# Performance work log

Hardware: AMD Instinct MI355X
Metric: run time of the kernel (lower is better)

## Reference

```python
import jax, jax.numpy as jnp
import numpy as np

B, S, E, H = 2, 2048, 1024, 16
D = E // H          # head_dim = 64
HK = H // 4         # heads per kernel group = 4
MASKED_BIAS = -10000.0


def _dwconv_causal(x, w, b):
    # x: [B, h, S, D], w: [D, k], b: [D]; causal depthwise conv along S
    k = w.shape[1]
    s = x.shape[2]
    xp = jnp.pad(x, ((0, 0), (0, 0), (k - 1, 0), (0, 0)))
    out = b
    for i in range(k):
        out = out + xp[:, :, i:i + s, :] * w[:, i]
    return out


def setup_inputs() -> dict:
    key = jax.random.key(0)
    ks = jax.random.split(key, 32)
    inp = {
        'hidden_states': jax.random.normal(ks[0], (B, S, E), jnp.float32),
        'c_attn_w': jax.random.normal(ks[1], (E, 3 * E), jnp.float32) * 0.02,
        'c_attn_b': jnp.zeros((3 * E,), jnp.float32),
        'c_proj_w': jax.random.normal(ks[2], (E, E), jnp.float32) * 0.02,
        'c_proj_b': jnp.zeros((E,), jnp.float32),
    }
    i = 3
    for pre in ('q', 'k', 'v'):
        for kern in (3, 5, 7):
            inp[f'{pre}w{kern}'] = jax.random.normal(ks[i], (D, kern), jnp.float32) * (1.0 / kern)
            inp[f'{pre}b{kern}'] = jnp.zeros((D,), jnp.float32)
            i += 1
    return inp


def _forward(hidden_states, c_attn_w, c_attn_b, c_proj_w, c_proj_b,
             qw3, qb3, qw5, qb5, qw7, qb7,
             kw3, kb3, kw5, kb5, kw7, kb7,
             vw3, vb3, vw5, vb5, vw7, vb7):
    qkv = hidden_states @ c_attn_w + c_attn_b            # [B,S,3E]
    q, k, v = jnp.split(qkv, 3, axis=-1)

    def split_heads(t):
        return t.reshape(B, S, H, D).transpose(0, 2, 1, 3)  # [B,H,S,D]

    q, k, v = split_heads(q), split_heads(k), split_heads(v)

    def tranception_mix(t, ws_bs):
        parts = [t[:, :HK]]
        for g, (w, b) in enumerate(ws_bs):
            parts.append(_dwconv_causal(t[:, (g + 1) * HK:(g + 2) * HK], w, b))
        return jnp.concatenate(parts, axis=1)

    q = tranception_mix(q, [(qw3, qb3), (qw5, qb5), (qw7, qb7)])
    k = tranception_mix(k, [(kw3, kb3), (kw5, kb5), (kw7, kb7)])
    v = tranception_mix(v, [(vw3, vb3), (vw5, vb5), (vw7, vb7)])

    scores = jnp.einsum('bhqd,bhkd->bhqk', q, k) / jnp.sqrt(jnp.float32(D))
    causal = jnp.tril(jnp.ones((S, S), bool))
    scores = jnp.where(causal, scores, jnp.float32(MASKED_BIAS))
    attn = jax.nn.softmax(scores, axis=-1)
    out = jnp.einsum('bhqk,bhkd->bhqd', attn, v)
    out = out.transpose(0, 2, 1, 3).reshape(B, S, E)
    return out @ c_proj_w + c_proj_b


def reference(hidden_states, c_attn_w, c_attn_b, c_proj_w, c_proj_b,
              qw3, qb3, qw5, qb5, qw7, qb7,
              kw3, kb3, kw5, kb5, kw7, kb7,
              vw3, vb3, vw5, vb5, vw7, vb7):
    return _forward(hidden_states, c_attn_w, c_attn_b, c_proj_w, c_proj_b,
                    qw3, qb3, qw5, qb5, qw7, qb7,
                    kw3, kb3, kw5, kb5, kw7, kb7,
                    vw3, vb3, vw5, vb5, vw7, vb7)
```

## Files before the change

### kernel.cpp

```cpp
#include <hip/hip_runtime.h>
#include <stdint.h>
#include <math.h>

typedef unsigned short u16;
typedef __attribute__((ext_vector_type(8))) short short8;
typedef __attribute__((ext_vector_type(4))) float floatx4;

#define DEV static __device__ __forceinline__

struct alignas(8) us4 { u16 x, y, z, w; };
struct alignas(16) us8 { u16 v[8]; };
struct alignas(16) f4 { float x, y, z, w; };
struct alignas(8) f2 { float x, y; };
struct alignas(8) u32x2 { uint32_t x, y; };

DEV u16 f2bf(float f) {
  uint32_t u = __float_as_uint(f);
  u += 0x7fffu + ((u >> 16) & 1u);
  return (u16)(u >> 16);
}
DEV float bf2f(u16 h) { return __uint_as_float(((uint32_t)h) << 16); }

DEV uint32_t pkbf(float a, float b) {
#if __has_builtin(__builtin_amdgcn_cvt_pk_bf16_f32)
  typedef __attribute__((ext_vector_type(2))) __bf16 bf2_t;
  bf2_t v = __builtin_amdgcn_cvt_pk_bf16_f32(a, b);
  uint32_t r; __builtin_memcpy(&r, &v, 4); return r;
#else
  return (uint32_t)f2bf(a) | ((uint32_t)f2bf(b) << 16);
#endif
}

DEV float fexp2(float x) {
#if __has_builtin(__builtin_amdgcn_exp2f)
  return __builtin_amdgcn_exp2f(x);
#else
  return exp2f(x);
#endif
}

DEV void load_lds16(const void* g, void* l) {
  __builtin_amdgcn_global_load_lds((const __attribute__((address_space(1))) void*)g,
                                   (__attribute__((address_space(3))) void*)l, 16, 0, 0);
}

__global__ __launch_bounds__(256) void prep_fused(const float* __restrict__ hidden, u16* __restrict__ h_bf,
                                                  const float* __restrict__ attn_w, u16* __restrict__ wqkvT,
                                                  const float* __restrict__ proj_w, u16* __restrict__ wprojT) {
  __shared__ float tile[32][33];
  const int bx = blockIdx.x;
  const int t = threadIdx.x;
  if (bx < 4096) {
    const int i = (bx * 256 + t) * 4;
    f4 v = *(const f4*)(hidden + i);
    us4 o; o.x = f2bf(v.x); o.y = f2bf(v.y); o.z = f2bf(v.z); o.w = f2bf(v.w);
    *(us4*)(h_bf + i) = o;
    return;
  }
  const float* in; u16* out; int K, N, n0, k0;
  if (bx < 7168) {
    const int bid = bx - 4096;
    in = attn_w; out = wqkvT; K = 1024; N = 3072;
    n0 = (bid % 96) * 32; k0 = (bid / 96) * 32;
  } else {
    const int bid = bx - 7168;
    in = proj_w; out = wprojT; K = 1024; N = 1024;
    n0 = (bid & 31) * 32; k0 = (bid >> 5) * 32;
  }
  const int tx = t & 31, ty = t >> 5;
  for (int i = ty; i < 32; i += 8)
    tile[i][tx] = in[(size_t)(k0 + i) * N + n0 + tx];
  __syncthreads();
  for (int i = ty; i < 32; i += 8)
    out[(size_t)(n0 + i) * K + k0 + tx] = f2bf(tile[tx][i]);
}

template <int EPI, int BN, int NGRP>
__global__ __launch_bounds__(256) void gemm_bt(const u16* __restrict__ A,
                                               const u16* __restrict__ Bt,
                                               const float* __restrict__ bias,
                                               void* __restrict__ outp,
                                               int M, int N, int K) {
  constexpr int NT = BN / 32;
  __shared__ u16 lA[128 * 64];
  __shared__ u16 lB[BN * 64];
  const int t = threadIdx.x;
  const int w = t >> 6, lane = t & 63;
  const int quad = lane >> 4, l15 = lane & 15;
  const int wm = w >> 1, wn = w & 1;
  const int wn_off = wn * (BN / 2);

  const int bid = blockIdx.x;
  const int gsz = 32 * NGRP;
  const int grp = bid / gsz;
  const int r = bid - grp * gsz;
  const int m0 = (r & 31) * 128;
  const int n0 = (grp * NGRP + (r >> 5)) * BN;

  floatx4 acc[4][NT] = {};

  const int srow = t >> 3;
  const int scol = (((t & 7) ^ (srow & 7)) << 3);
  const u16* gA = A + (size_t)(m0 + srow) * K + scol;
  const u16* gB = Bt + (size_t)(n0 + srow) * K + scol;
  u16* sA = lA + t * 8;
  u16* sB = lB + t * 8;
  const size_t rstep = (size_t)32 * K;

  for (int k0 = 0; k0 < K; k0 += 64) {
#pragma unroll
    for (int c = 0; c < 4; c++) load_lds16(gA + c * rstep, sA + c * 2048);
#pragma unroll
    for (int c = 0; c < BN / 32; c++) load_lds16(gB + c * rstep, sB + c * 2048);
    gA += 64; gB += 64;
    __syncthreads();
#pragma unroll
    for (int kc = 0; kc < 2; kc++) {
      short8 af[4], bfr[NT];
#pragma unroll
      for (int mt = 0; mt < 4; mt++)
        af[mt] = *(const short8*)&lA[(wm * 64 + mt * 16 + l15) * 64 + (((kc * 4 + quad) ^ (l15 & 7)) << 3)];
#pragma unroll
      for (int nt = 0; nt < NT; nt++)
        bfr[nt] = *(const short8*)&lB[(wn_off + nt * 16 + l15) * 64 + (((kc * 4 + quad) ^ (l15 & 7)) << 3)];
#pragma unroll
      for (int mt = 0; mt < 4; mt++)
#pragma unroll
        for (int nt = 0; nt < NT; nt++)
          acc[mt][nt] = __builtin_amdgcn_mfma_f32_16x16x32_bf16(bfr[nt], af[mt], acc[mt][nt], 0, 0, 0);
    }
    __syncthreads();
  }

  if (EPI == 0) {
    u16* outq = (u16*)outp;
#pragma unroll
    for (int nt = 0; nt < NT; nt++) {
      const int nb = n0 + wn_off + nt * 16 + quad * 4;
      const f4 bn4 = *(const f4*)&bias[nb];
      const int tensor = nb >> 10, e = nb & 1023;
      const int h = e >> 6, d = e & 63;
      const size_t abase = (size_t)tensor * 4194304 + (size_t)h * 131072 + d;
#pragma unroll
      for (int mt = 0; mt < 4; mt++) {
        const int rr = m0 + wm * 64 + mt * 16 + l15;
        const int b = rr >> 11, s = rr & 2047;
        u32x2 o;
        o.x = pkbf(acc[mt][nt][0] + bn4.x, acc[mt][nt][1] + bn4.y);
        o.y = pkbf(acc[mt][nt][2] + bn4.z, acc[mt][nt][3] + bn4.w);
        *(u32x2*)&outq[abase + (size_t)b * 2097152 + (size_t)s * 64] = o;
      }
    }
  } else {
    float* outf = (float*)outp;
#pragma unroll
    for (int nt = 0; nt < NT; nt++) {
      const int nb = n0 + wn_off + nt * 16 + quad * 4;
      const f4 bn4 = *(const f4*)&bias[nb];
#pragma unroll
      for (int mt = 0; mt < 4; mt++) {
        const int rr = m0 + wm * 64 + mt * 16 + l15;
        f4 o;
        o.x = acc[mt][nt][0] + bn4.x;
        o.y = acc[mt][nt][1] + bn4.y;
        o.z = acc[mt][nt][2] + bn4.z;
        o.w = acc[mt][nt][3] + bn4.w;
        *(f4*)&outf[(size_t)rr * N + nb] = o;
      }
    }
  }
}

struct ConvW { const float* w[9]; const float* b[9]; };

template <int K>
DEV void conv_run(const u16* xt, int sl0, int d, const float* wp, const float* bp,
                  float qscale, float* out32) {
  float wr[K];
#pragma unroll
  for (int j = 0; j < K; j++) wr[j] = wp[d * K + j];
  const float br = bp[d];
  float win[K];
#pragma unroll
  for (int m = 1; m < K; m++) win[m] = bf2f(xt[(sl0 + 6 - K + m) * 68 + d]);
#pragma unroll
  for (int i = 0; i < 32; i++) {
#pragma unroll
    for (int m = 0; m < K - 1; m++) win[m] = win[m + 1];
    win[K - 1] = bf2f(xt[(sl0 + 6 + i) * 68 + d]);
    float val = br;
#pragma unroll
    for (int j = 0; j < K; j++) val += wr[j] * win[j];
    out32[i] = val * qscale;
  }
}

__global__ __launch_bounds__(256) void conv_mix(const u16* __restrict__ qkv, ConvW cw,
                                                u16* __restrict__ qpost,
                                                u16* __restrict__ kpost,
                                                u16* __restrict__ vpostT) {
  __shared__ u16 xt[134 * 68];
  __shared__ u16 yt[64 * 136];
  const int t = threadIdx.x;
  const int s0 = blockIdx.x * 128;
  const int h = blockIdx.y;
  const int tz = blockIdx.z;
  const int tensor = tz >> 1, b = tz & 1;
  const u16* src = qkv + (((size_t)tensor * 2 + b) * 16 + h) * 131072;

  for (int idx = t; idx < 134 * 16; idx += 256) {
    const int row = idx >> 4, c4 = (idx & 15) << 2;
    const int s = s0 - 6 + row;
    us4 v = {0, 0, 0, 0};
    if (s >= 0) v = *(const us4*)&src[(size_t)s * 64 + c4];
    *(us4*)&xt[row * 68 + c4] = v;
  }
  __syncthreads();

  const int group = h >> 2;
  const float* wp = (group > 0) ? cw.w[tensor * 3 + group - 1] : nullptr;
  const float* bp = (group > 0) ? cw.b[tensor * 3 + group - 1] : nullptr;
  const float qscale = (tensor == 0) ? 0.18033688f : 1.0f;

  const int d = t & 63;
  const int sl0 = (t >> 6) * 32;

  float out32[32];
  if (group == 0) {
#pragma unroll
    for (int i = 0; i < 32; i++)
      out32[i] = bf2f(xt[(sl0 + 6 + i) * 68 + d]) * qscale;
  } else if (group == 1) {
    conv_run<3>(xt, sl0, d, wp, bp, qscale, out32);
  } else if (group == 2) {
    conv_run<5>(xt, sl0, d, wp, bp, qscale, out32);
  } else {
    conv_run<7>(xt, sl0, d, wp, bp, qscale, out32);
  }

  if (tensor < 2) {
    u16* outp = (tensor == 0) ? qpost : kpost;
    const size_t ob = (((size_t)b * 16 + h) * 2048 + s0) * 64;
#pragma unroll
    for (int i = 0; i < 32; i++)
      outp[ob + (size_t)(sl0 + i) * 64 + d] = f2bf(out32[i]);
  } else {
#pragma unroll
    for (int i = 0; i < 32; i++)
      yt[d * 136 + sl0 + i] = f2bf(out32[i]);
    __syncthreads();
    const size_t ob = ((size_t)b * 16 + h) * 64;
    const int sl = (t & 15) * 8;
#pragma unroll
    for (int pass = 0; pass < 4; pass++) {
      const int dd = (t >> 4) + pass * 16;
      us8 vv = *(const us8*)&yt[dd * 136 + sl];
      *(us8*)&vpostT[(ob + dd) * 2048 + s0 + sl] = vv;
    }
  }
}

__global__ __launch_bounds__(256) void attn_fwd(const u16* __restrict__ Q,
                                                const u16* __restrict__ Kp,
                                                const u16* __restrict__ Vt,
                                                u16* __restrict__ Out,
                                                u16* __restrict__ Opart,
                                                f2* __restrict__ ml) {
  __shared__ u16 lK[2][128 * 64];
  __shared__ u16 lV[2][64 * 128];
  __shared__ u16 lP[4][32 * 64];
  const int t = threadIdx.x;
  const int w = t >> 6, lane = t & 63;
  const int quad = lane >> 4, l15 = lane & 15;
  const int e7 = l15 & 7;

  const int lin = blockIdx.x;
  const int xcd = lin & 7;
  const int idx = lin >> 3;
  const int grp = idx / 72;
  const int u = idx - grp * 72;
  const int bh = grp * 8 + xcd;
  int p = (int)(0.5f * (sqrtf(4.0f * (float)u + 1.0f) - 1.0f));
  if ((p + 1) * (p + 2) <= u) p++;
  if (p * (p + 1) > u) p--;
  const int v = u - p * (p + 1);
  const int qi = 2 * p + (v >= p + 1 ? 1 : 0);
  const int slab = v - (v >= p + 1 ? p + 1 : 0);
  const int ns = (qi + 2) >> 1;
  const int jbeg = slab * 2;
  const int nh = min(2, qi + 1 - jbeg);

  const int b = bh >> 4, h = bh & 15;
  const size_t qkbase = (size_t)bh * 131072;
  const int qblk = qi * 128 + w * 32;

  short8 qf[2][2];
#pragma unroll
  for (int qt = 0; qt < 2; qt++)
#pragma unroll
    for (int kc = 0; kc < 2; kc++)
      qf[qt][kc] = *(const short8*)&Q[qkbase + (size_t)(qblk + qt * 16 + l15) * 64 + kc * 32 + quad * 8];

  float mst[2] = {-3.0e38f, -3.0e38f};
  float lst[2] = {0.0f, 0.0f};
  floatx4 accO[4][2] = {};

  const int krow = t >> 3;
  const int kcol = (((t & 7) ^ (krow & 7)) << 3);
  const u16* gK = Kp + qkbase + (size_t)krow * 64 + kcol;
  const int vrow = t >> 4;
  const int vcol = (((t & 15) ^ vrow) << 3);
  const u16* gV = Vt + qkbase + (size_t)vrow * 2048 + vcol;
  u16* myP = lP[w];

  for (int hf = 0; hf < nh; hf++) {
    const int j0 = (jbeg + hf) * 128;
    u16* sK = &lK[hf][0] + t * 8;
    u16* sV = &lV[hf][0] + t * 8;
#pragma unroll
    for (int c = 0; c < 4; c++) {
      load_lds16(gK + (size_t)(j0 + c * 32) * 64, sK + c * 2048);
      load_lds16(gV + j0 + c * 16 * 2048, sV + c * 2048);
    }
  }
  __syncthreads();

  for (int hf = 0; hf < nh; hf++) {
    const int j = jbeg + hf;
    const int j0 = j * 128;
    const u16* cK = lK[hf];
    const u16* cV = lV[hf];

    floatx4 accS[8][2] = {};
#pragma unroll
    for (int kvt = 0; kvt < 8; kvt++) {
#pragma unroll
      for (int kc = 0; kc < 2; kc++) {
        const short8 a = *(const short8*)&cK[(kvt * 16 + l15) * 64 + (((kc * 4 + quad) ^ e7) << 3)];
#pragma unroll
        for (int qt = 0; qt < 2; qt++)
          accS[kvt][qt] = __builtin_amdgcn_mfma_f32_16x16x32_bf16(a, qf[qt][kc], accS[kvt][qt], 0, 0, 0);
      }
    }

    if (j == qi) {
#pragma unroll
      for (int qt = 0; qt < 2; qt++) {
        const int q = qblk + qt * 16 + l15;
#pragma unroll
        for (int kvt = 0; kvt < 8; kvt++)
#pragma unroll
          for (int r = 0; r < 4; r++) {
            const int kv = j0 + kvt * 16 + quad * 4 + r;
            if (kv > q) accS[kvt][qt][r] = -3.0e38f;
          }
      }
    }

    uint32_t pk01[2][8], pk23[2][8];
    float alpha[2];
#pragma unroll
    for (int qt = 0; qt < 2; qt++) {
      float tm = -3.0e38f;
#pragma unroll
      for (int kvt = 0; kvt < 8; kvt++)
#pragma unroll
        for (int r = 0; r < 4; r++)
          tm = fmaxf(tm, accS[kvt][qt][r]);
      tm = fmaxf(tm, __shfl_xor(tm, 16));
      tm = fmaxf(tm, __shfl_xor(tm, 32));
      const float mnew = fmaxf(mst[qt], tm);
      alpha[qt] = fexp2(mst[qt] - mnew);
      mst[qt] = mnew;
      float ts = 0.0f;
#pragma unroll
      for (int kvt = 0; kvt < 8; kvt++) {
        const float p0 = fexp2(accS[kvt][qt][0] - mnew);
        const float p1 = fexp2(accS[kvt][qt][1] - mnew);
        const float p2 = fexp2(accS[kvt][qt][2] - mnew);
        const float p3 = fexp2(accS[kvt][qt][3] - mnew);
        ts += (p0 + p1) + (p2 + p3);
        pk01[qt][kvt] = pkbf(p0, p1);
        pk23[qt][kvt] = pkbf(p2, p3);
      }
      ts += __shfl_xor(ts, 16);
      ts += __shfl_xor(ts, 32);
      lst[qt] = lst[qt] * alpha[qt] + ts;
    }

#pragma unroll
    for (int dt = 0; dt < 4; dt++)
#pragma unroll
      for (int qt = 0; qt < 2; qt++)
#pragma unroll
        for (int r = 0; r < 4; r++)
          accO[dt][qt][r] *= alpha[qt];

#pragma unroll
    for (int kvh = 0; kvh < 2; kvh++) {
#pragma unroll
      for (int qt = 0; qt < 2; qt++) {
        const int prow = (qt * 16 + l15) * 64;
#pragma unroll
        for (int kt = 0; kt < 4; kt++) {
          const int kvt = kvh * 4 + kt;
          const int slot = (kt * 2 + (quad >> 1)) ^ e7;
          u32x2 pk; pk.x = pk01[qt][kvt]; pk.y = pk23[qt][kvt];
          *(u32x2*)&myP[prow + slot * 8 + (quad & 1) * 4] = pk;
        }
      }
      asm volatile("s_waitcnt lgkmcnt(0)" ::: "memory");
#pragma unroll
      for (int kk = 0; kk < 2; kk++) {
        const int kvc = kvh * 2 + kk;
        short8 pf[2];
#pragma unroll
        for (int qt = 0; qt < 2; qt++)
          pf[qt] = *(const short8*)&myP[(qt * 16 + l15) * 64 + (((kk * 4 + quad) ^ e7) << 3)];
#pragma unroll
        for (int dt = 0; dt < 4; dt++) {
          const short8 vf = *(const short8*)&cV[(dt * 16 + l15) * 128 + (((kvc * 4 + quad) ^ l15) << 3)];
#pragma unroll
          for (int qt = 0; qt < 2; qt++)
            accO[dt][qt] = __builtin_amdgcn_mfma_f32_16x16x32_bf16(vf, pf[qt], accO[dt][qt], 0, 0, 0);
        }
      }
    }
  }

  if (ns == 1) {
#pragma unroll
    for (int qt = 0; qt < 2; qt++) {
      const float inv = 1.0f / lst[qt];
      const int q = qblk + qt * 16 + l15;
#pragma unroll
      for (int dt = 0; dt < 4; dt++) {
        u32x2 o;
        o.x = pkbf(accO[dt][qt][0] * inv, accO[dt][qt][1] * inv);
        o.y = pkbf(accO[dt][qt][2] * inv, accO[dt][qt][3] * inv);
        *(u32x2*)&Out[((size_t)b * 2048 + q) * 1024 + h * 64 + dt * 16 + quad * 4] = o;
      }
    }
  } else {
    const int slot = bh * 72 + u;
    u16* op = Opart + (size_t)slot * 8192;
#pragma unroll
    for (int qt = 0; qt < 2; qt++) {
      const int ql = w * 32 + qt * 16 + l15;
#pragma unroll
      for (int dt = 0; dt < 4; dt++) {
        u32x2 o;
        o.x = pkbf(accO[dt][qt][0], accO[dt][qt][1]);
        o.y = pkbf(accO[dt][qt][2], accO[dt][qt][3]);
        *(u32x2*)&op[(size_t)ql * 64 + dt * 16 + quad * 4] = o;
      }
      if (quad == 0) {
        f2 v2; v2.x = mst[qt]; v2.y = lst[qt];
        ml[slot * 128 + ql] = v2;
      }
    }
  }
}

__global__ __launch_bounds__(256) void attn_reduce(const u16* __restrict__ Opart,
                                                   const f2* __restrict__ ml,
                                                   u16* __restrict__ Out) {
  const int qi = blockIdx.x + 2;
  const int bh = blockIdx.y;
  const int b = bh >> 4, h = bh & 15;
  const int p = qi >> 1;
  const int base = bh * 72 + p * (p + 1) + (qi & 1) * (p + 1);
  const int ns = (qi + 2) >> 1;
  const int t = threadIdx.x;
  const int q = t >> 1, dh = (t & 1) * 32;

  float m[8], l[8], wgt[8];
  float mmax = -3.0e38f;
  for (int s = 0; s < ns; s++) {
    f2 v = ml[(base + s) * 128 + q];
    m[s] = v.x; l[s] = v.y;
    mmax = fmaxf(mmax, m[s]);
  }
  float lsum = 0.0f;
  for (int s = 0; s < ns; s++) {
    wgt[s] = fexp2(m[s] - mmax);
    lsum += wgt[s] * l[s];
  }
  float acc[32] = {};
  for (int s = 0; s < ns; s++) {
    const u16* src = Opart + ((size_t)(base + s) * 128 + q) * 64 + dh;
    const float ws = wgt[s];
#pragma unroll
    for (int i = 0; i < 8; i++) {
      us4 vv = *(const us4*)&src[i * 4];
      acc[i * 4 + 0] += ws * bf2f(vv.x);
      acc[i * 4 + 1] += ws * bf2f(vv.y);
      acc[i * 4 + 2] += ws * bf2f(vv.z);
      acc[i * 4 + 3] += ws * bf2f(vv.w);
    }
  }
  const float inv = 1.0f / lsum;
  u16* dst = Out + ((size_t)b * 2048 + qi * 128 + q) * 1024 + h * 64 + dh;
#pragma unroll
  for (int i = 0; i < 8; i++) {
    u32x2 o;
    o.x = pkbf(acc[i * 4 + 0] * inv, acc[i * 4 + 1] * inv);
    o.y = pkbf(acc[i * 4 + 2] * inv, acc[i * 4 + 3] * inv);
    *(u32x2*)&dst[i * 4] = o;
  }
}

extern "C" void kernel_launch(void* const* d_in, const int* in_sizes, int n_in,
                              void* d_out, int out_size, void* d_ws, size_t ws_size,
                              hipStream_t stream) {
  (void)in_sizes; (void)n_in; (void)out_size; (void)ws_size;
  const float* hidden = (const float*)d_in[0];
  const float* attn_w = (const float*)d_in[1];
  const float* attn_b = (const float*)d_in[2];
  const float* proj_w = (const float*)d_in[3];
  const float* proj_b = (const float*)d_in[4];
  ConvW cw;
  for (int i = 0; i < 9; i++) {
    cw.w[i] = (const float*)d_in[5 + 2 * i];
    cw.b[i] = (const float*)d_in[6 + 2 * i];
  }

  uint8_t* ws = (uint8_t*)d_ws;
  u16* h_bf   = (u16*)(ws + 0);
  u16* wqkvT  = (u16*)(ws + 8388608);
  u16* qkvpre = (u16*)(ws + 14680064);
  u16* qpost  = (u16*)(ws + 39845888);
  u16* kpost  = (u16*)(ws + 48234496);
  u16* vpostT = (u16*)(ws + 56623104);
  u16* attno  = (u16*)(ws + 65011712);
  u16* wprojT = (u16*)(ws + 73400320);
  f2*  ml     = (f2*) (ws + 75497472);
  u16* Opart  = (u16*)(ws + 0);

  prep_fused<<<8192, 256, 0, stream>>>(hidden, h_bf, attn_w, wqkvT, proj_w, wprojT);
  gemm_bt<0, 128, 6><<<768, 256, 0, stream>>>(h_bf, wqkvT, attn_b, (void*)qkvpre, 4096, 3072, 1024);
  conv_mix<<<dim3(16, 16, 6), 256, 0, stream>>>(qkvpre, cw, qpost, kpost, vpostT);
  attn_fwd<<<dim3(2304), 256, 0, stream>>>(qpost, kpost, vpostT, attno, Opart, ml);
  attn_reduce<<<dim3(14, 32), 256, 0, stream>>>(Opart, ml, attno);
  gemm_bt<1, 64, 8><<<512, 256, 0, stream>>>(attno, wprojT, proj_b, d_out, 4096, 1024, 1024);
}
```

Before: 250.7 us.

## Load K/V MFMA fragments directly from global memory instead of LDS staging

Removes the shared-memory staging buffers for K and V tiles in the attention kernel and has each wave read its MFMA operand fragments straight from global memory into registers. The LDS footprint drops to just the P buffer, and launch bounds now request 3 blocks per CU for higher occupancy. The cost is that the four waves of a block each fetch the same K/V data redundantly, relying on L1/L2 cache hits, with more scattered 16-byte global loads and higher global-load latency exposure.

```diff
diff --git a/kernel.cpp b/kernel.cpp
--- a/kernel.cpp
+++ b/kernel.cpp
@@ -260,14 +260,12 @@
   }
 }
 
-__global__ __launch_bounds__(256) void attn_fwd(const u16* __restrict__ Q,
-                                                const u16* __restrict__ Kp,
-                                                const u16* __restrict__ Vt,
-                                                u16* __restrict__ Out,
-                                                u16* __restrict__ Opart,
-                                                f2* __restrict__ ml) {
-  __shared__ u16 lK[2][128 * 64];
-  __shared__ u16 lV[2][64 * 128];
+__global__ __launch_bounds__(256, 3) void attn_fwd(const u16* __restrict__ Q,
+                                                   const u16* __restrict__ Kp,
+                                                   const u16* __restrict__ Vt,
+                                                   u16* __restrict__ Out,
+                                                   u16* __restrict__ Opart,
+                                                   f2* __restrict__ ml) {
   __shared__ u16 lP[4][32 * 64];
   const int t = threadIdx.x;
   const int w = t >> 6, lane = t & 63;
@@ -305,42 +303,26 @@
   float lst[2] = {0.0f, 0.0f};
   floatx4 accO[4][2] = {};
 
-  const int krow = t >> 3;
-  const int kcol = (((t & 7) ^ (krow & 7)) << 3);
-  const u16* gK = Kp + qkbase + (size_t)krow * 64 + kcol;
-  const int vrow = t >> 4;
-  const int vcol = (((t & 15) ^ vrow) << 3);
-  const u16* gV = Vt + qkbase + (size_t)vrow * 2048 + vcol;
+  const u16* pK = Kp + qkbase + (size_t)l15 * 64 + quad * 8;
+  const u16* pV = Vt + qkbase + (size_t)l15 * 2048 + quad * 8;
   u16* myP = lP[w];
-
-  for (int hf = 0; hf < nh; hf++) {
-    const int j0 = (jbeg + hf) * 128;
-    u16* sK = &lK[hf][0] + t * 8;
-    u16* sV = &lV[hf][0] + t * 8;
-#pragma unroll
-    for (int c = 0; c < 4; c++) {
-      load_lds16(gK + (size_t)(j0 + c * 32) * 64, sK + c * 2048);
-      load_lds16(gV + j0 + c * 16 * 2048, sV + c * 2048);
-    }
-  }
-  __syncthreads();
 
   for (int hf = 0; hf < nh; hf++) {
     const int j = jbeg + hf;
     const int j0 = j * 128;
-    const u16* cK = lK[hf];
-    const u16* cV = lV[hf];
 
     floatx4 accS[8][2] = {};
 #pragma unroll
-    for (int kvt = 0; kvt < 8; kvt++) {
-#pragma unroll
-      for (int kc = 0; kc < 2; kc++) {
-        const short8 a = *(const short8*)&cK[(kvt * 16 + l15) * 64 + (((kc * 4 + quad) ^ e7) << 3)];
+    for (int kc = 0; kc < 2; kc++) {
+      short8 af[8];
+#pragma unroll
+      for (int kvt = 0; kvt < 8; kvt++)
+        af[kvt] = *(const short8*)&pK[(size_t)(j0 + kvt * 16) * 64 + kc * 32];
+#pragma unroll
+      for (int kvt = 0; kvt < 8; kvt++)
 #pragma unroll
         for (int qt = 0; qt < 2; qt++)
-          accS[kvt][qt] = __builtin_amdgcn_mfma_f32_16x16x32_bf16(a, qf[qt][kc], accS[kvt][qt], 0, 0, 0);
-      }
+          accS[kvt][qt] = __builtin_amdgcn_mfma_f32_16x16x32_bf16(af[kvt], qf[qt][kc], accS[kvt][qt], 0, 0, 0);
     }
 
     if (j == qi) {
@@ -398,6 +380,12 @@
 
 #pragma unroll
     for (int kvh = 0; kvh < 2; kvh++) {
+      short8 vfr[2][4];
+#pragma unroll
+      for (int kk = 0; kk < 2; kk++)
+#pragma unroll
+        for (int dt = 0; dt < 4; dt++)
+          vfr[kk][dt] = *(const short8*)&pV[(size_t)(dt * 16) * 2048 + j0 + (kvh * 2 + kk) * 32];
 #pragma unroll
       for (int qt = 0; qt < 2; qt++) {
         const int prow = (qt * 16 + l15) * 64;
@@ -412,18 +400,15 @@
       asm volatile("s_waitcnt lgkmcnt(0)" ::: "memory");
 #pragma unroll
       for (int kk = 0; kk < 2; kk++) {
-        const int kvc = kvh * 2 + kk;
         short8 pf[2];
 #pragma unroll
         for (int qt = 0; qt < 2; qt++)
           pf[qt] = *(const short8*)&myP[(qt * 16 + l15) * 64 + (((kk * 4 + quad) ^ e7) << 3)];
 #pragma unroll
-        for (int dt = 0; dt < 4; dt++) {
-          const short8 vf = *(const short8*)&cV[(dt * 16 + l15) * 128 + (((kvc * 4 + quad) ^ l15) << 3)];
+        for (int dt = 0; dt < 4; dt++)
 #pragma unroll
           for (int qt = 0; qt < 2; qt++)
-            accO[dt][qt] = __builtin_amdgcn_mfma_f32_16x16x32_bf16(vf, pf[qt], accO[dt][qt], 0, 0, 0);
-        }
+            accO[dt][qt] = __builtin_amdgcn_mfma_f32_16x16x32_bf16(vfr[kk][dt], pf[qt], accO[dt][qt], 0, 0, 0);
       }
     }
   }
```

After: 281.6 us. 12.3% more time.
